# Kernel tuning notes

Measured on AMD Instinct MI355X. Metric: run time of the kernel, lower is better.

The kernel has to match this reference:

```python
import jax, jax.numpy as jnp
import numpy as np

NUM_HEADS = 4
NUM_GROUPS = 8
EPS = 1e-5


def setup_inputs() -> dict:
    key = jax.random.key(0)
    ks = jax.random.split(key, 4)
    B, C, H, W = 4, 256, 64, 64
    x = jax.random.normal(ks[0], (B, C, H, W), dtype=jnp.float32)
    gamma = jnp.ones((C,), dtype=jnp.float32)
    beta = jnp.zeros((C,), dtype=jnp.float32)
    w_qkv = jax.random.normal(ks[1], (3 * C, C), dtype=jnp.float32) * 0.02
    b_qkv = jnp.zeros((3 * C,), dtype=jnp.float32)
    w_proj = jax.random.normal(ks[2], (C, C), dtype=jnp.float32) * 0.02
    b_proj = jnp.zeros((C,), dtype=jnp.float32)
    return {"x": x, "gamma": gamma, "beta": beta, "w_qkv": w_qkv,
            "b_qkv": b_qkv, "w_proj": w_proj, "b_proj": b_proj}


def _group_norm(x, gamma, beta):
    B, C, H, W = x.shape
    xg = x.reshape(B, NUM_GROUPS, C // NUM_GROUPS, H, W)
    mean = xg.mean(axis=(2, 3, 4), keepdims=True)
    var = xg.var(axis=(2, 3, 4), keepdims=True)
    xn = ((xg - mean) * jax.lax.rsqrt(var + EPS)).reshape(B, C, H, W)
    return xn * gamma[None, :, None, None] + beta[None, :, None, None]


def reference(x, gamma, beta, w_qkv, b_qkv, w_proj, b_proj):
    B, C, H, W = x.shape
    d = C // NUM_HEADS
    scale = d ** (-0.5)
    xn = _group_norm(x, gamma, beta)
    # 1x1 conv == per-pixel linear: (B,C,H,W) x (3C,C) -> (B,3C,H,W)
    qkv = jnp.einsum('bchw,oc->bohw', xn, w_qkv) + b_qkv[None, :, None, None]
    q, k, v = jnp.split(qkv, 3, axis=1)
    S = H * W
    q = q.reshape(B, NUM_HEADS, d, S)  # (B,h,d,S)
    k = k.reshape(B, NUM_HEADS, d, S)
    v = v.reshape(B, NUM_HEADS, d, S)
    # attn scores: q^T k, scaled AFTER the matmul (as in source)
    attn = jax.nn.softmax(jnp.einsum('bhds,bhdt->bhst', q, k) * scale, axis=-1)
    # out = attn @ v^T -> (B,h,S,d) then transpose to (B,h,d,S) -> (B,C,H,W)
    out = jnp.einsum('bhst,bhdt->bhds', attn, v).reshape(B, C, H, W)
    y = jnp.einsum('bchw,oc->bohw', out, w_proj) + b_proj[None, :, None, None]
    return x + y
```

## Files before the change

kernel.cpp:

```cpp
#include <hip/hip_runtime.h>
#include <hip/hip_bf16.h>


typedef __attribute__((ext_vector_type(8))) short          b16x8;
typedef __attribute__((ext_vector_type(4))) float          f32x4;
typedef __attribute__((ext_vector_type(4))) unsigned short u16x4;
typedef __attribute__((ext_vector_type(8))) unsigned short u16x8;

#define SWZ(row, chunk) (((chunk) ^ ((row) & 7)))

__device__ __forceinline__ unsigned short f2bf(float f) {
    union { float f; unsigned u; } v; v.f = f;
    unsigned r = v.u + 0x7FFF + ((v.u >> 16) & 1);
    return (unsigned short)(r >> 16);
}

__device__ __forceinline__ float bf2f(unsigned short u) {
    union { unsigned u; float f; } v; v.u = ((unsigned)u) << 16;
    return v.f;
}

__device__ __forceinline__ unsigned bfpack_trunc(float lo, float hi) {
    union { float f; unsigned u; } a, b;
    a.f = hi; b.f = lo;
    return __builtin_amdgcn_perm(a.u, b.u, 0x07060302u);
}

__device__ __forceinline__ float fexp2(float x) {
#if __has_builtin(__builtin_amdgcn_exp2f)
    return __builtin_amdgcn_exp2f(x);
#else
    return exp2f(x);
#endif
}

__device__ __forceinline__ void gll16(const void* g, void* l) {
    __builtin_amdgcn_global_load_lds(
        (const __attribute__((address_space(1))) unsigned int*)g,
        (__attribute__((address_space(3))) unsigned int*)l, 16, 0, 0);
}

__global__ __launch_bounds__(256) void prepack(const float* __restrict__ wqkv,
                                               const float* __restrict__ bqkv,
                                               unsigned short* __restrict__ wsw,
                                               float* __restrict__ bq_pre) {
    int gid = blockIdx.x * 256 + threadIdx.x;
    const float qs = 0.125f * 1.44269504f;
    int o = gid >> 5, ch = gid & 31, cblk = ch >> 3, chl = ch & 7;
    float sc = (o < 256) ? qs : 1.f;
    const float* src = &wqkv[o * 256 + ch * 8];
    u16x8 v;
    for (int i = 0; i < 8; i++) v[i] = f2bf(src[i] * sc);
    *(u16x8*)&wsw[((cblk * 768 + o) << 6) + SWZ(o, chl) * 8] = v;
    if (gid < 768) bq_pre[gid] = bqkv[gid] * ((gid < 256) ? qs : 1.f);
}

__global__ __launch_bounds__(256) void gn_partial(const float* __restrict__ x,
                                                  float* __restrict__ partials) {
    int bx = blockIdx.x;
    int bg = bx >> 4, part = bx & 15;
    const float* xp = x + (size_t)bg * 131072 + (size_t)part * 8192;
    int t = threadIdx.x;
    float s = 0.f, ss = 0.f;
    for (int k = 0; k < 8; k++) {
        float4 v = *(const float4*)(xp + t * 4 + k * 1024);
        s += v.x + v.y + v.z + v.w;
        ss += v.x * v.x + v.y * v.y + v.z * v.z + v.w * v.w;
    }
    for (int off = 32; off; off >>= 1) {
        s += __shfl_down(s, off);
        ss += __shfl_down(ss, off);
    }
    __shared__ float rs[4], rss[4];
    if ((t & 63) == 0) { rs[t >> 6] = s; rss[t >> 6] = ss; }
    __syncthreads();
    if (t == 0) {
        partials[2 * bx]     = rs[0] + rs[1] + rs[2] + rs[3];
        partials[2 * bx + 1] = rss[0] + rss[1] + rss[2] + rss[3];
    }
}

__global__ __launch_bounds__(64) void gn_final(const float* __restrict__ partials,
                                               float* __restrict__ stats) {
    int bg = threadIdx.x;
    if (bg < 32) {
        float s = 0.f, ss = 0.f;
        for (int p = 0; p < 16; p++) {
            s  += partials[2 * (bg * 16 + p)];
            ss += partials[2 * (bg * 16 + p) + 1];
        }
        const float invN = 1.f / 131072.f;
        float mean = s * invN;
        float var = ss * invN - mean * mean;
        stats[2 * bg] = mean;
        stats[2 * bg + 1] = rsqrtf(var + 1e-5f);
    }
}

__global__ __launch_bounds__(256) void qkv_gemm(const float* __restrict__ x,
                                                const float* __restrict__ gamma,
                                                const float* __restrict__ beta,
                                                const unsigned short* __restrict__ wsw,
                                                const float* __restrict__ bq_pre,
                                                const float* __restrict__ stats,
                                                unsigned short* __restrict__ qT,
                                                unsigned short* __restrict__ kT,
                                                unsigned short* __restrict__ vT) {
    __shared__ __align__(16) unsigned short Asm[256 * 64];
    __shared__ __align__(16) unsigned short Bsm[64 * 72];
    int s0 = blockIdx.x * 64, sec = blockIdx.y, b = blockIdx.z;
    int t = threadIdx.x, lane = t & 63, wv = t >> 6;
    int l15 = lane & 15, quad = lane >> 4;
    f32x4 acc[4][4] = {};

    int tc = t >> 5;
    int ts = (t & 31) * 2;

    for (int k0 = 0; k0 < 256; k0 += 64) {
        int cblk = k0 >> 6;
        __syncthreads();
        const unsigned short* asrc = wsw + (((size_t)cblk * 768 + sec * 256) << 6);
        for (int j = 0; j < 8; j++) {
            int blk = wv * 8 + j;
            gll16(asrc + blk * 512 + lane * 8, &Asm[blk * 512]);
        }
        {
            int cbase = k0 + tc * 8;
            int g = cbase >> 5;
            float mean = stats[2 * (b * 8 + g)], rstd = stats[2 * (b * 8 + g) + 1];
            u16x8 r0, r1;
            for (int ci = 0; ci < 8; ci++) {
                int c = cbase + ci;
                float2 xv = *(const float2*)&x[((size_t)(b * 256 + c)) * 4096 + s0 + ts];
                float ga = gamma[c] * rstd, be = beta[c] - mean * gamma[c] * rstd;
                r0[ci] = (short)f2bf(xv.x * ga + be);
                r1[ci] = (short)f2bf(xv.y * ga + be);
            }
            *(u16x8*)&Bsm[(ts + 0) * 72 + tc * 8] = r0;
            *(u16x8*)&Bsm[(ts + 1) * 72 + tc * 8] = r1;
        }
        __syncthreads();
        for (int kc = 0; kc < 2; kc++) {
            b16x8 bb[4];
            for (int nn = 0; nn < 4; nn++)
                bb[nn] = *(const b16x8*)(Bsm + (nn * 16 + l15) * 72 + kc * 32 + quad * 8);
            for (int ot = 0; ot < 4; ot++) {
                int row = wv * 16 + l15;
                b16x8 a = *(const b16x8*)&Asm[(ot * 64 + row) * 64 + SWZ(row, kc * 4 + quad) * 8];
                for (int nn = 0; nn < 4; nn++)
                    acc[ot][nn] = __builtin_amdgcn_mfma_f32_16x16x32_bf16(a, bb[nn], acc[ot][nn], 0, 0, 0);
            }
        }
    }

    if (sec < 2) {
        unsigned short* dstT = (sec == 0) ? qT : kT;
        for (int ot = 0; ot < 4; ot++) {
            __syncthreads();
            for (int nn = 0; nn < 4; nn++) {
                u16x4 pv;
                for (int r = 0; r < 4; r++) {
                    int o = sec * 256 + ot * 64 + wv * 16 + quad * 4 + r;
                    pv[r] = f2bf(acc[ot][nn][r] + bq_pre[o]);
                }
                *(u16x4*)&Bsm[(nn * 16 + l15) * 72 + wv * 16 + quad * 4] = pv;
            }
            __syncthreads();
            unsigned short* dst = dstT + (size_t)(b * 4 + ot) * 4096 * 64;
            int s_l = t >> 2;
            for (int j = 0; j < 2; j++) {
                int cp = (t & 3) * 2 + j;
                u16x8 val = *(u16x8*)&Bsm[s_l * 72 + cp * 8];
                *(u16x8*)&dst[(size_t)(s0 + s_l) * 64 + SWZ(s_l, cp) * 8] = val;
            }
        }
    } else {
        int kt = blockIdx.x;
        for (int ot = 0; ot < 4; ot++) {
            int bh = b * 4 + ot;
            for (int r = 0; r < 4; r++) {
                int dd = wv * 16 + quad * 4 + r;
                float bs = bq_pre[512 + ot * 64 + dd];
                u16x4 pv = { f2bf(acc[ot][0][r] + bs), f2bf(acc[ot][1][r] + bs),
                             f2bf(acc[ot][2][r] + bs), f2bf(acc[ot][3][r] + bs) };
                size_t off = ((size_t)(bh * 64 + kt) * 64 + dd) * 64
                           + SWZ(dd, l15 >> 1) * 8 + (l15 & 1) * 4;
                *(u16x4*)&vT[off] = pv;
            }
        }
    }
}

__global__ __launch_bounds__(256) void attn_kernel(const unsigned short* __restrict__ qT,
                                                   const unsigned short* __restrict__ kT,
                                                   const unsigned short* __restrict__ vT,
                                                   unsigned short* __restrict__ Opart,
                                                   float* __restrict__ lsum) {
    __shared__ __align__(16) unsigned short QP[128 * 64];
    __shared__ __align__(16) unsigned short KV[2][2][64 * 64];
    int bx = blockIdx.x;
    int q0 = (bx >> 1) * 128;
    int half = bx & 1;
    int kt0 = half * 32, ktN = kt0 + 32;
    int h = blockIdx.y, b = blockIdx.z;
    int bh = b * 4 + h, slab = bh * 2 + half;
    int t = threadIdx.x, lane = t & 63, wv = t >> 6;
    int l15 = lane & 15, quad = lane >> 4;

    const unsigned short* qTb = qT + (size_t)bh * 4096 * 64;
    const unsigned short* kTb = kT + (size_t)bh * 4096 * 64;
    const unsigned short* vTb = vT + (size_t)bh * 64 * 4096;

    for (int j = 0; j < 8; j++) {
        int i = wv + 4 * j;
        if (i < 16) {
            gll16(qTb + (size_t)q0 * 64 + i * 512 + lane * 8, &QP[i * 512]);
        } else if (i < 24) {
            int ii = i - 16;
            gll16(kTb + (size_t)kt0 * 4096 + ii * 512 + lane * 8, &KV[0][0][ii * 512]);
        } else {
            int ii = i - 24;
            gll16(vTb + (size_t)kt0 * 4096 + ii * 512 + lane * 8, &KV[0][1][ii * 512]);
        }
    }
    __syncthreads();

    b16x8 aq[2][2];
    for (int mt = 0; mt < 2; mt++)
        for (int kc = 0; kc < 2; kc++) {
            int row = wv * 32 + mt * 16 + l15;
            aq[mt][kc] = *(const b16x8*)&QP[row * 64 + SWZ(row, kc * 4 + quad) * 8];
        }

    f32x4 O[2][4] = {};
    float ls[2][4] = {};

    for (int kt = kt0; kt < ktN; kt++) {
        int cur = kt & 1;
        if (kt < ktN - 1) {
            int nb = cur ^ 1;
            for (int j = 0; j < 4; j++) {
                int i = wv + 4 * j;
                int which = i >> 3, ii = i & 7;
                const unsigned short* src = (which == 0)
                    ? kTb + (size_t)(kt + 1) * 4096 + ii * 512 + lane * 8
                    : vTb + (size_t)(kt + 1) * 4096 + ii * 512 + lane * 8;
                gll16(src, &KV[nb][which][ii * 512]);
            }
        }

        f32x4 sc[2][4] = {};
        for (int kc = 0; kc < 2; kc++) {
            b16x8 bk[4];
            for (int nk = 0; nk < 4; nk++) {
                int row = nk * 16 + l15;
                bk[nk] = *(const b16x8*)&KV[cur][0][row * 64 + SWZ(l15, kc * 4 + quad) * 8];
            }
            for (int mt = 0; mt < 2; mt++)
                for (int nk = 0; nk < 4; nk++)
                    sc[mt][nk] = __builtin_amdgcn_mfma_f32_16x16x32_bf16(
                        aq[mt][kc], bk[nk], sc[mt][nk], 0, 0, 0);
        }

        for (int mt = 0; mt < 2; mt++) {
            for (int r = 0; r < 4; r++) {
                float p0 = fexp2(sc[mt][0][r]);
                float p1 = fexp2(sc[mt][1][r]);
                float p2 = fexp2(sc[mt][2][r]);
                float p3 = fexp2(sc[mt][3][r]);
                ls[mt][r] += (p0 + p1) + (p2 + p3);
                int row = wv * 32 + mt * 16 + quad * 4 + r;
                unsigned lo = bfpack_trunc(p0, p1);
                unsigned hi = bfpack_trunc(p2, p3);
                uint2 pk = { lo, hi };
                *(uint2*)&QP[row * 64 + SWZ(row, l15 >> 1) * 8 + (l15 & 1) * 4] = pk;
            }
        }

        for (int kc = 0; kc < 2; kc++) {
            b16x8 ap[2], bv[4];
            for (int mt = 0; mt < 2; mt++) {
                int row = wv * 32 + mt * 16 + l15;
                ap[mt] = *(const b16x8*)&QP[row * 64 + SWZ(row, kc * 4 + quad) * 8];
            }
            for (int nf = 0; nf < 4; nf++) {
                int row = nf * 16 + l15;
                bv[nf] = *(const b16x8*)&KV[cur][1][row * 64 + SWZ(l15, kc * 4 + quad) * 8];
            }
            for (int mt = 0; mt < 2; mt++)
                for (int nf = 0; nf < 4; nf++)
                    O[mt][nf] = __builtin_amdgcn_mfma_f32_16x16x32_bf16(
                        ap[mt], bv[nf], O[mt][nf], 0, 0, 0);
        }

        __syncthreads();
    }

    for (int mt = 0; mt < 2; mt++)
        for (int r = 0; r < 4; r++) {
            float s = ls[mt][r];
            for (int off = 1; off < 16; off <<= 1) s += __shfl_xor(s, off);
            int srow = q0 + wv * 32 + mt * 16 + quad * 4 + r;
            if (l15 == 0) lsum[(size_t)slab * 4096 + srow] = s;
        }

    for (int mt = 0; mt < 2; mt++)
        for (int nf = 0; nf < 4; nf++)
            for (int r = 0; r < 4; r++) {
                int s = q0 + wv * 32 + mt * 16 + quad * 4 + r;
                int d = nf * 16 + l15;
                Opart[((size_t)slab * 4096 + s) * 64 + d] = f2bf(O[mt][nf][r]);
            }
}

__global__ __launch_bounds__(256) void attn_combine(const unsigned short* __restrict__ Opart,
                                                    const float* __restrict__ lsum,
                                                    unsigned short* __restrict__ aout) {
    int gid = blockIdx.x * 256 + threadIdx.x;
    int bh = gid >> 16;
    int rem = gid & 65535;
    int s = rem >> 4;
    int d4 = (rem & 15) * 4;
    int b = bh >> 2, h = bh & 3;
    size_t base0 = ((size_t)(bh * 2 + 0) * 4096 + s) * 64 + d4;
    size_t base1 = ((size_t)(bh * 2 + 1) * 4096 + s) * 64 + d4;
    u16x4 o0 = *(const u16x4*)&Opart[base0];
    u16x4 o1 = *(const u16x4*)&Opart[base1];
    float l0 = lsum[(size_t)(bh * 2 + 0) * 4096 + s];
    float l1 = lsum[(size_t)(bh * 2 + 1) * 4096 + s];
    float rcp = 1.f / (l0 + l1);
    u16x4 res;
    for (int j = 0; j < 4; j++)
        res[j] = f2bf((bf2f(o0[j]) + bf2f(o1[j])) * rcp);
    *(u16x4*)&aout[((size_t)b * 4096 + s) * 256 + h * 64 + d4] = res;
}

__global__ __launch_bounds__(256) void proj_gemm(const unsigned short* __restrict__ aout,
                                                 const float* __restrict__ w,
                                                 const float* __restrict__ bias,
                                                 const float* __restrict__ x,
                                                 float* __restrict__ out) {
    __shared__ __align__(16) unsigned short Asm[64 * 72];
    __shared__ __align__(16) unsigned short Bsm[64 * 72];
    int s0 = blockIdx.x * 64, o0 = blockIdx.y * 64, b = blockIdx.z;
    int t = threadIdx.x, lane = t & 63, wv = t >> 6;
    int l15 = lane & 15, quad = lane >> 4;
    int rl = t >> 2;
    f32x4 acc[4] = {};
    for (int k0 = 0; k0 < 256; k0 += 64) {
        __syncthreads();
        for (int j = 0; j < 4; j++) {
            int c4 = (t & 3) * 16 + j * 4;
            float4 w4 = *(const float4*)&w[(size_t)(o0 + rl) * 256 + k0 + c4];
            u16x4 p = { f2bf(w4.x), f2bf(w4.y), f2bf(w4.z), f2bf(w4.w) };
            *(u16x4*)&Asm[rl * 72 + c4] = p;
        }
        for (int j = 0; j < 2; j++) {
            int c = (t & 3) * 16 + j * 8;
            u16x8 v = *(const u16x8*)&aout[((size_t)b * 4096 + s0 + rl) * 256 + k0 + c];
            *(u16x8*)&Bsm[rl * 72 + c] = v;
        }
        __syncthreads();
        for (int kc = 0; kc < 2; kc++) {
            b16x8 a = *(const b16x8*)(Asm + (wv * 16 + l15) * 72 + kc * 32 + quad * 8);
            for (int nn = 0; nn < 4; nn++) {
                b16x8 bb = *(const b16x8*)(Bsm + (nn * 16 + l15) * 72 + kc * 32 + quad * 8);
                acc[nn] = __builtin_amdgcn_mfma_f32_16x16x32_bf16(a, bb, acc[nn], 0, 0, 0);
            }
        }
    }
    for (int nn = 0; nn < 4; nn++) {
        for (int r = 0; r < 4; r++) {
            int o = o0 + wv * 16 + quad * 4 + r;
            int s = s0 + nn * 16 + l15;
            size_t idx = ((size_t)(b * 256 + o)) * 4096 + s;
            out[idx] = acc[nn][r] + bias[o] + x[idx];
        }
    }
}

extern "C" void kernel_launch(void* const* d_in, const int* in_sizes, int n_in,
                              void* d_out, int out_size, void* d_ws, size_t ws_size,
                              hipStream_t stream) {
    const float* x      = (const float*)d_in[0];
    const float* gamma  = (const float*)d_in[1];
    const float* beta   = (const float*)d_in[2];
    const float* w_qkv  = (const float*)d_in[3];
    const float* b_qkv  = (const float*)d_in[4];
    const float* w_proj = (const float*)d_in[5];
    const float* b_proj = (const float*)d_in[6];
    float* out = (float*)d_out;

    unsigned short* ws = (unsigned short*)d_ws;
    unsigned short* qT    = ws;
    unsigned short* kT    = qT + (size_t)16 * 4096 * 64;
    unsigned short* vT    = kT + (size_t)16 * 4096 * 64;
    unsigned short* aout  = vT + (size_t)16 * 4096 * 64;
    unsigned short* Opart = aout + (size_t)4 * 4096 * 256;
    float*          lsump = (float*)(Opart + (size_t)32 * 4096 * 64);
    unsigned short* wqkv_sw = (unsigned short*)lsump;
    float*          bq_pre  = (float*)((char*)lsump + 393216);
    float* stats    = (float*)aout;
    float* partials = stats + 64;

    hipLaunchKernelGGL(prepack,      dim3(96),       dim3(256), 0, stream,
                       w_qkv, b_qkv, wqkv_sw, bq_pre);
    hipLaunchKernelGGL(gn_partial,   dim3(512),      dim3(256), 0, stream, x, partials);
    hipLaunchKernelGGL(gn_final,     dim3(1),        dim3(64),  0, stream, partials, stats);
    hipLaunchKernelGGL(qkv_gemm,     dim3(64, 3, 4), dim3(256), 0, stream,
                       x, gamma, beta, wqkv_sw, bq_pre, stats, qT, kT, vT);
    hipLaunchKernelGGL(attn_kernel,  dim3(64, 4, 4), dim3(256), 0, stream,
                       qT, kT, vT, Opart, lsump);
    hipLaunchKernelGGL(attn_combine, dim3(4096),     dim3(256), 0, stream,
                       Opart, lsump, aout);
    hipLaunchKernelGGL(proj_gemm,    dim3(64, 4, 4), dim3(256), 0, stream,
                       aout, w_proj, b_proj, x, out);
}
```

Before: 213.3 us.

## Fuse GN/prepack, fold stats and attention combine into consumers, MFMA row sums

```diff
diff --git a/kernel.cpp b/kernel.cpp
--- a/kernel.cpp
+++ b/kernel.cpp
@@ -34,66 +34,58 @@
 #endif
 }
 
+__device__ __forceinline__ float frcp(float x) {
+#if __has_builtin(__builtin_amdgcn_rcpf)
+    return __builtin_amdgcn_rcpf(x);
+#else
+    return 1.f / x;
+#endif
+}
+
 __device__ __forceinline__ void gll16(const void* g, void* l) {
     __builtin_amdgcn_global_load_lds(
         (const __attribute__((address_space(1))) unsigned int*)g,
         (__attribute__((address_space(3))) unsigned int*)l, 16, 0, 0);
 }
 
-__global__ __launch_bounds__(256) void prepack(const float* __restrict__ wqkv,
-                                               const float* __restrict__ bqkv,
-                                               unsigned short* __restrict__ wsw,
-                                               float* __restrict__ bq_pre) {
-    int gid = blockIdx.x * 256 + threadIdx.x;
-    const float qs = 0.125f * 1.44269504f;
-    int o = gid >> 5, ch = gid & 31, cblk = ch >> 3, chl = ch & 7;
-    float sc = (o < 256) ? qs : 1.f;
-    const float* src = &wqkv[o * 256 + ch * 8];
-    u16x8 v;
-    for (int i = 0; i < 8; i++) v[i] = f2bf(src[i] * sc);
-    *(u16x8*)&wsw[((cblk * 768 + o) << 6) + SWZ(o, chl) * 8] = v;
-    if (gid < 768) bq_pre[gid] = bqkv[gid] * ((gid < 256) ? qs : 1.f);
-}
-
-__global__ __launch_bounds__(256) void gn_partial(const float* __restrict__ x,
-                                                  float* __restrict__ partials) {
+__global__ __launch_bounds__(256) void gn_prepack(const float* __restrict__ x,
+                                                  float* __restrict__ partials,
+                                                  const float* __restrict__ wqkv,
+                                                  const float* __restrict__ bqkv,
+                                                  unsigned short* __restrict__ wsw,
+                                                  float* __restrict__ bq_pre) {
     int bx = blockIdx.x;
-    int bg = bx >> 4, part = bx & 15;
-    const float* xp = x + (size_t)bg * 131072 + (size_t)part * 8192;
     int t = threadIdx.x;
-    float s = 0.f, ss = 0.f;
-    for (int k = 0; k < 8; k++) {
-        float4 v = *(const float4*)(xp + t * 4 + k * 1024);
-        s += v.x + v.y + v.z + v.w;
-        ss += v.x * v.x + v.y * v.y + v.z * v.z + v.w * v.w;
-    }
-    for (int off = 32; off; off >>= 1) {
-        s += __shfl_down(s, off);
-        ss += __shfl_down(ss, off);
-    }
-    __shared__ float rs[4], rss[4];
-    if ((t & 63) == 0) { rs[t >> 6] = s; rss[t >> 6] = ss; }
-    __syncthreads();
-    if (t == 0) {
-        partials[2 * bx]     = rs[0] + rs[1] + rs[2] + rs[3];
-        partials[2 * bx + 1] = rss[0] + rss[1] + rss[2] + rss[3];
-    }
-}
-
-__global__ __launch_bounds__(64) void gn_final(const float* __restrict__ partials,
-                                               float* __restrict__ stats) {
-    int bg = threadIdx.x;
-    if (bg < 32) {
+    if (bx < 512) {
+        int bg = bx >> 4, part = bx & 15;
+        const float* xp = x + (size_t)bg * 131072 + (size_t)part * 8192;
         float s = 0.f, ss = 0.f;
-        for (int p = 0; p < 16; p++) {
-            s  += partials[2 * (bg * 16 + p)];
-            ss += partials[2 * (bg * 16 + p) + 1];
-        }
-        const float invN = 1.f / 131072.f;
-        float mean = s * invN;
-        float var = ss * invN - mean * mean;
-        stats[2 * bg] = mean;
-        stats[2 * bg + 1] = rsqrtf(var + 1e-5f);
+        for (int k = 0; k < 8; k++) {
+            float4 v = *(const float4*)(xp + t * 4 + k * 1024);
+            s += v.x + v.y + v.z + v.w;
+            ss += v.x * v.x + v.y * v.y + v.z * v.z + v.w * v.w;
+        }
+        for (int off = 32; off; off >>= 1) {
+            s += __shfl_down(s, off);
+            ss += __shfl_down(ss, off);
+        }
+        __shared__ float rs[4], rss[4];
+        if ((t & 63) == 0) { rs[t >> 6] = s; rss[t >> 6] = ss; }
+        __syncthreads();
+        if (t == 0) {
+            partials[2 * bx]     = rs[0] + rs[1] + rs[2] + rs[3];
+            partials[2 * bx + 1] = rss[0] + rss[1] + rss[2] + rss[3];
+        }
+    } else {
+        int gid = (bx - 512) * 256 + t;
+        const float qs = 0.125f * 1.44269504f;
+        int o = gid >> 5, ch = gid & 31, cblk = ch >> 3, chl = ch & 7;
+        float sc = (o < 256) ? qs : 1.f;
+        const float* src = &wqkv[o * 256 + ch * 8];
+        u16x8 v;
+        for (int i = 0; i < 8; i++) v[i] = f2bf(src[i] * sc);
+        *(u16x8*)&wsw[((cblk * 768 + o) << 6) + SWZ(o, chl) * 8] = v;
+        if (gid < 768) bq_pre[gid] = bqkv[gid] * ((gid < 256) ? qs : 1.f);
     }
 }
 
@@ -102,17 +94,31 @@
                                                 const float* __restrict__ beta,
                                                 const unsigned short* __restrict__ wsw,
                                                 const float* __restrict__ bq_pre,
-                                                const float* __restrict__ stats,
+                                                const float* __restrict__ partials,
                                                 unsigned short* __restrict__ qT,
                                                 unsigned short* __restrict__ kT,
                                                 unsigned short* __restrict__ vT) {
     __shared__ __align__(16) unsigned short Asm[256 * 64];
     __shared__ __align__(16) unsigned short Bsm[64 * 72];
+    __shared__ float stats_s[16];
     int s0 = blockIdx.x * 64, sec = blockIdx.y, b = blockIdx.z;
     int t = threadIdx.x, lane = t & 63, wv = t >> 6;
     int l15 = lane & 15, quad = lane >> 4;
     f32x4 acc[4][4] = {};
 
+    if (t < 8) {
+        float s = 0.f, ss = 0.f;
+        for (int p = 0; p < 16; p++) {
+            s  += partials[2 * ((b * 8 + t) * 16 + p)];
+            ss += partials[2 * ((b * 8 + t) * 16 + p) + 1];
+        }
+        const float invN = 1.f / 131072.f;
+        float mean = s * invN;
+        float var = ss * invN - mean * mean;
+        stats_s[2 * t] = mean;
+        stats_s[2 * t + 1] = rsqrtf(var + 1e-5f);
+    }
+
     int tc = t >> 5;
     int ts = (t & 31) * 2;
 
@@ -127,7 +133,7 @@
         {
             int cbase = k0 + tc * 8;
             int g = cbase >> 5;
-            float mean = stats[2 * (b * 8 + g)], rstd = stats[2 * (b * 8 + g) + 1];
+            float mean = stats_s[2 * g], rstd = stats_s[2 * g + 1];
             u16x8 r0, r1;
             for (int ci = 0; ci < 8; ci++) {
                 int c = cbase + ci;
@@ -197,7 +203,8 @@
                                                    unsigned short* __restrict__ Opart,
                                                    float* __restrict__ lsum) {
     __shared__ __align__(16) unsigned short QP[128 * 64];
-    __shared__ __align__(16) unsigned short KV[2][2][64 * 64];
+    __shared__ __align__(16) unsigned short Ksm[2][64 * 64];
+    __shared__ __align__(16) unsigned short Vsm[64 * 64];
     int bx = blockIdx.x;
     int q0 = (bx >> 1) * 128;
     int half = bx & 1;
@@ -217,10 +224,10 @@
             gll16(qTb + (size_t)q0 * 64 + i * 512 + lane * 8, &QP[i * 512]);
         } else if (i < 24) {
             int ii = i - 16;
-            gll16(kTb + (size_t)kt0 * 4096 + ii * 512 + lane * 8, &KV[0][0][ii * 512]);
+            gll16(kTb + (size_t)kt0 * 4096 + ii * 512 + lane * 8, &Ksm[0][ii * 512]);
         } else {
             int ii = i - 24;
-            gll16(vTb + (size_t)kt0 * 4096 + ii * 512 + lane * 8, &KV[0][1][ii * 512]);
+            gll16(vTb + (size_t)kt0 * 4096 + ii * 512 + lane * 8, &Vsm[ii * 512]);
         }
     }
     __syncthreads();
@@ -232,21 +239,26 @@
             aq[mt][kc] = *(const b16x8*)&QP[row * 64 + SWZ(row, kc * 4 + quad) * 8];
         }
 
+    b16x8 ones;
+    for (int i = 0; i < 8; i++) ones[i] = (short)0x3F80;
+
     f32x4 O[2][4] = {};
-    float ls[2][4] = {};
+    f32x4 lsacc[2] = {};
 
     for (int kt = kt0; kt < ktN; kt++) {
         int cur = kt & 1;
-        if (kt < ktN - 1) {
-            int nb = cur ^ 1;
-            for (int j = 0; j < 4; j++) {
-                int i = wv + 4 * j;
-                int which = i >> 3, ii = i & 7;
-                const unsigned short* src = (which == 0)
-                    ? kTb + (size_t)(kt + 1) * 4096 + ii * 512 + lane * 8
-                    : vTb + (size_t)(kt + 1) * 4096 + ii * 512 + lane * 8;
-                gll16(src, &KV[nb][which][ii * 512]);
-            }
+        int nb = cur ^ 1;
+        u16x8 vpre0, vpre1;
+        bool more = (kt < ktN - 1);
+        if (more) {
+            for (int j = 0; j < 2; j++) {
+                int blk = wv * 2 + j;
+                gll16(kTb + (size_t)(kt + 1) * 4096 + blk * 512 + lane * 8,
+                      &Ksm[nb][blk * 512]);
+            }
+            const unsigned short* vsrc = vTb + (size_t)(kt + 1) * 4096;
+            vpre0 = *(const u16x8*)&vsrc[t * 8];
+            vpre1 = *(const u16x8*)&vsrc[2048 + t * 8];
         }
 
         f32x4 sc[2][4] = {};
@@ -254,7 +266,7 @@
             b16x8 bk[4];
             for (int nk = 0; nk < 4; nk++) {
                 int row = nk * 16 + l15;
-                bk[nk] = *(const b16x8*)&KV[cur][0][row * 64 + SWZ(l15, kc * 4 + quad) * 8];
+                bk[nk] = *(const b16x8*)&Ksm[cur][row * 64 + SWZ(l15, kc * 4 + quad) * 8];
             }
             for (int mt = 0; mt < 2; mt++)
                 for (int nk = 0; nk < 4; nk++)
@@ -268,11 +280,8 @@
                 float p1 = fexp2(sc[mt][1][r]);
                 float p2 = fexp2(sc[mt][2][r]);
                 float p3 = fexp2(sc[mt][3][r]);
-                ls[mt][r] += (p0 + p1) + (p2 + p3);
                 int row = wv * 32 + mt * 16 + quad * 4 + r;
-                unsigned lo = bfpack_trunc(p0, p1);
-                unsigned hi = bfpack_trunc(p2, p3);
-                uint2 pk = { lo, hi };
+                uint2 pk = { bfpack_trunc(p0, p1), bfpack_trunc(p2, p3) };
                 *(uint2*)&QP[row * 64 + SWZ(row, l15 >> 1) * 8 + (l15 & 1) * 4] = pk;
             }
         }
@@ -285,23 +294,29 @@
             }
             for (int nf = 0; nf < 4; nf++) {
                 int row = nf * 16 + l15;
-                bv[nf] = *(const b16x8*)&KV[cur][1][row * 64 + SWZ(l15, kc * 4 + quad) * 8];
-            }
-            for (int mt = 0; mt < 2; mt++)
+                bv[nf] = *(const b16x8*)&Vsm[row * 64 + SWZ(l15, kc * 4 + quad) * 8];
+            }
+            for (int mt = 0; mt < 2; mt++) {
+                lsacc[mt] = __builtin_amdgcn_mfma_f32_16x16x32_bf16(
+                    ap[mt], ones, lsacc[mt], 0, 0, 0);
                 for (int nf = 0; nf < 4; nf++)
                     O[mt][nf] = __builtin_amdgcn_mfma_f32_16x16x32_bf16(
                         ap[mt], bv[nf], O[mt][nf], 0, 0, 0);
-        }
-
-        __syncthreads();
+            }
+        }
+
+        __syncthreads();
+        if (more) {
+            *(u16x8*)&Vsm[t * 8]        = vpre0;
+            *(u16x8*)&Vsm[2048 + t * 8] = vpre1;
+            __syncthreads();
+        }
     }
 
     for (int mt = 0; mt < 2; mt++)
         for (int r = 0; r < 4; r++) {
-            float s = ls[mt][r];
-            for (int off = 1; off < 16; off <<= 1) s += __shfl_xor(s, off);
             int srow = q0 + wv * 32 + mt * 16 + quad * 4 + r;
-            if (l15 == 0) lsum[(size_t)slab * 4096 + srow] = s;
+            if (l15 == 0) lsum[(size_t)slab * 4096 + srow] = lsacc[mt][r];
         }
 
     for (int mt = 0; mt < 2; mt++)
@@ -313,29 +328,8 @@
             }
 }
 
-__global__ __launch_bounds__(256) void attn_combine(const unsigned short* __restrict__ Opart,
-                                                    const float* __restrict__ lsum,
-                                                    unsigned short* __restrict__ aout) {
-    int gid = blockIdx.x * 256 + threadIdx.x;
-    int bh = gid >> 16;
-    int rem = gid & 65535;
-    int s = rem >> 4;
-    int d4 = (rem & 15) * 4;
-    int b = bh >> 2, h = bh & 3;
-    size_t base0 = ((size_t)(bh * 2 + 0) * 4096 + s) * 64 + d4;
-    size_t base1 = ((size_t)(bh * 2 + 1) * 4096 + s) * 64 + d4;
-    u16x4 o0 = *(const u16x4*)&Opart[base0];
-    u16x4 o1 = *(const u16x4*)&Opart[base1];
-    float l0 = lsum[(size_t)(bh * 2 + 0) * 4096 + s];
-    float l1 = lsum[(size_t)(bh * 2 + 1) * 4096 + s];
-    float rcp = 1.f / (l0 + l1);
-    u16x4 res;
-    for (int j = 0; j < 4; j++)
-        res[j] = f2bf((bf2f(o0[j]) + bf2f(o1[j])) * rcp);
-    *(u16x4*)&aout[((size_t)b * 4096 + s) * 256 + h * 64 + d4] = res;
-}
-
-__global__ __launch_bounds__(256) void proj_gemm(const unsigned short* __restrict__ aout,
+__global__ __launch_bounds__(256) void proj_gemm(const unsigned short* __restrict__ Opart,
+                                                 const float* __restrict__ lsum,
                                                  const float* __restrict__ w,
                                                  const float* __restrict__ bias,
                                                  const float* __restrict__ x,
@@ -355,10 +349,22 @@
             u16x4 p = { f2bf(w4.x), f2bf(w4.y), f2bf(w4.z), f2bf(w4.w) };
             *(u16x4*)&Asm[rl * 72 + c4] = p;
         }
-        for (int j = 0; j < 2; j++) {
-            int c = (t & 3) * 16 + j * 8;
-            u16x8 v = *(const u16x8*)&aout[((size_t)b * 4096 + s0 + rl) * 256 + k0 + c];
-            *(u16x8*)&Bsm[rl * 72 + c] = v;
+        {
+            int hh = k0 >> 6;
+            int bh = b * 4 + hh;
+            int s = s0 + rl;
+            float l0 = lsum[(size_t)(bh * 2 + 0) * 4096 + s];
+            float l1 = lsum[(size_t)(bh * 2 + 1) * 4096 + s];
+            float rcp = frcp(l0 + l1);
+            for (int j = 0; j < 2; j++) {
+                int off = (t & 3) * 16 + j * 8;
+                u16x8 o0v = *(const u16x8*)&Opart[((size_t)(bh * 2 + 0) * 4096 + s) * 64 + off];
+                u16x8 o1v = *(const u16x8*)&Opart[((size_t)(bh * 2 + 1) * 4096 + s) * 64 + off];
+                u16x8 res;
+                for (int i = 0; i < 8; i++)
+                    res[i] = f2bf((bf2f(o0v[i]) + bf2f(o1v[i])) * rcp);
+                *(u16x8*)&Bsm[rl * 72 + off] = res;
+            }
         }
         __syncthreads();
         for (int kc = 0; kc < 2; kc++) {
@@ -395,24 +401,19 @@
     unsigned short* qT    = ws;
     unsigned short* kT    = qT + (size_t)16 * 4096 * 64;
     unsigned short* vT    = kT + (size_t)16 * 4096 * 64;
-    unsigned short* aout  = vT + (size_t)16 * 4096 * 64;
-    unsigned short* Opart = aout + (size_t)4 * 4096 * 256;
+    unsigned short* scratch = vT + (size_t)16 * 4096 * 64;
+    unsigned short* Opart = scratch + (size_t)4 * 4096 * 256;
     float*          lsump = (float*)(Opart + (size_t)32 * 4096 * 64);
     unsigned short* wqkv_sw = (unsigned short*)lsump;
     float*          bq_pre  = (float*)((char*)lsump + 393216);
-    float* stats    = (float*)aout;
-    float* partials = stats + 64;
-
-    hipLaunchKernelGGL(prepack,      dim3(96),       dim3(256), 0, stream,
-                       w_qkv, b_qkv, wqkv_sw, bq_pre);
-    hipLaunchKernelGGL(gn_partial,   dim3(512),      dim3(256), 0, stream, x, partials);
-    hipLaunchKernelGGL(gn_final,     dim3(1),        dim3(64),  0, stream, partials, stats);
-    hipLaunchKernelGGL(qkv_gemm,     dim3(64, 3, 4), dim3(256), 0, stream,
-                       x, gamma, beta, wqkv_sw, bq_pre, stats, qT, kT, vT);
-    hipLaunchKernelGGL(attn_kernel,  dim3(64, 4, 4), dim3(256), 0, stream,
+    float*          partials = (float*)scratch;
+
+    hipLaunchKernelGGL(gn_prepack,  dim3(608),      dim3(256), 0, stream,
+                       x, partials, w_qkv, b_qkv, wqkv_sw, bq_pre);
+    hipLaunchKernelGGL(qkv_gemm,    dim3(64, 3, 4), dim3(256), 0, stream,
+                       x, gamma, beta, wqkv_sw, bq_pre, partials, qT, kT, vT);
+    hipLaunchKernelGGL(attn_kernel, dim3(64, 4, 4), dim3(256), 0, stream,
                        qT, kT, vT, Opart, lsump);
-    hipLaunchKernelGGL(attn_combine, dim3(4096),     dim3(256), 0, stream,
-                       Opart, lsump, aout);
-    hipLaunchKernelGGL(proj_gemm,    dim3(64, 4, 4), dim3(256), 0, stream,
-                       aout, w_proj, b_proj, x, out);
-}
+    hipLaunchKernelGGL(proj_gemm,   dim3(64, 4, 4), dim3(256), 0, stream,
+                       Opart, lsump, w_proj, b_proj, x, out);
+}
```

Result: faster. 194.8 us (-8.7%).
